# Optimization experiments

Hardware: AMD Instinct MI355X
Metric: run time of the kernel (lower is better)

## Reference

```python
import jax, jax.numpy as jnp
import numpy as np

D_MODEL = 512
NUM_HEADS = 8
DEPTH = D_MODEL // NUM_HEADS
BATCH = 2
SEQ = 2048
NEG_INF_SCALE = -1e9


def setup_inputs() -> dict:
    key = jax.random.key(0)
    ks = jax.random.split(key, 9)
    s = 0.02
    return {
        "v": jax.random.normal(ks[0], (BATCH, SEQ, D_MODEL), jnp.float32),
        "q": jax.random.normal(ks[1], (BATCH, SEQ, D_MODEL), jnp.float32),
        "k": jax.random.normal(ks[2], (BATCH, SEQ, D_MODEL), jnp.float32),
        "mask": jax.random.randint(ks[3], (BATCH, 1, SEQ, SEQ), 0, 2, jnp.int32),
        "wq_w": jax.random.normal(ks[4], (D_MODEL, D_MODEL), jnp.float32) * s,
        "wq_b": jnp.zeros((D_MODEL,), jnp.float32),
        "wk_w": jax.random.normal(ks[5], (D_MODEL, D_MODEL), jnp.float32) * s,
        "wk_b": jnp.zeros((D_MODEL,), jnp.float32),
        "wv_w": jax.random.normal(ks[6], (D_MODEL, D_MODEL), jnp.float32) * s,
        "wv_b": jnp.zeros((D_MODEL,), jnp.float32),
        "wo_w": jax.random.normal(ks[7], (D_MODEL, D_MODEL), jnp.float32) * s,
        "wo_b": jnp.zeros((D_MODEL,), jnp.float32),
    }


def _split_heads(x, b):
    # [b, s, d_model] -> [b, h, s, depth]
    return x.reshape(b, -1, NUM_HEADS, DEPTH).transpose(0, 2, 1, 3)


def reference(v, q, k, mask, wq_w, wq_b, wk_w, wk_b, wv_w, wv_b, wo_w, wo_b):
    b = q.shape[0]
    vv = _split_heads(v @ wv_w + wv_b, b)  # [b,h,s,d]
    kk = _split_heads(k @ wk_w + wk_b, b)
    qq = _split_heads(q @ wq_w + wq_b, b)
    # NOTE: the original code swaps q/k at the helper call site, so logits = K @ Q^T.
    logits = jnp.einsum("bhkd,bhqd->bhkq", kk, qq) / jnp.sqrt(jnp.float32(DEPTH))
    logits = logits + mask.astype(jnp.float32) * NEG_INF_SCALE
    attn = jax.nn.softmax(logits, axis=-1)  # softmax over the query axis (faithful quirk)
    # output = A^T @ V  -> [b,h,q,d]
    out = jnp.einsum("bhkq,bhkd->bhqd", attn, vv)
    concat = out.transpose(0, 2, 1, 3).reshape(b, -1, D_MODEL)
    return concat @ wo_w + wo_b, attn
```

## Files before the change

### kernel.cpp

```cpp
#include <hip/hip_runtime.h>

#define S 2048
#define DM 512
#define NH 8
#define HD 64
#define NB 2
#define BH (NB * NH)
#define MROWS (NB * S)

typedef __bf16 bf16x8 __attribute__((ext_vector_type(8)));
typedef float f32x4 __attribute__((ext_vector_type(4)));

union FragU {
  uint4 u;
  bf16x8 v;
  unsigned short s[8];
};

__device__ __forceinline__ unsigned short f2bf(float x) {
  unsigned u = __float_as_uint(x);
  u += 0x7FFFu + ((u >> 16) & 1u);
  return (unsigned short)(u >> 16);
}

__global__ void k_wtrans(const float* __restrict__ w0, const float* __restrict__ w1,
                         const float* __restrict__ w2, const float* __restrict__ w3,
                         unsigned short* __restrict__ wt) {
  __shared__ float tile[64][65];
  int i = blockIdx.z;
  const float* w = (i == 0) ? w0 : (i == 1) ? w1 : (i == 2) ? w2 : w3;
  int k0 = blockIdx.x * 64;
  int n0 = blockIdx.y * 64;
  int tx = threadIdx.x, ty = threadIdx.y;
  for (int r = ty; r < 64; r += 4)
    tile[r][tx] = w[(size_t)(k0 + r) * DM + n0 + tx];
  __syncthreads();
  unsigned short* o = wt + (size_t)i * DM * DM;
  for (int r = ty; r < 64; r += 4)
    o[(size_t)(n0 + r) * DM + k0 + tx] = f2bf(tile[tx][r]);
}

__global__ __launch_bounds__(256) void k_proj(
    const float* __restrict__ inq, const float* __restrict__ ink, const float* __restrict__ inv,
    const unsigned short* __restrict__ wt,
    const float* __restrict__ bq, const float* __restrict__ bk, const float* __restrict__ bv,
    unsigned short* __restrict__ oq, unsigned short* __restrict__ ok, unsigned short* __restrict__ ov) {
  int which = blockIdx.z;
  const float* in = (which == 0) ? inq : (which == 1) ? ink : inv;
  const float* bias = (which == 0) ? bq : (which == 1) ? bk : bv;
  unsigned short* out = (which == 0) ? oq : (which == 1) ? ok : ov;
  const unsigned short* w = wt + (size_t)which * DM * DM;

  int lane = threadIdx.x & 63, wv = threadIdx.x >> 6;
  int m0 = blockIdx.x * 64 + wv * 16;
  int n0 = blockIdx.y * 64;
  int kf = (lane >> 4) * 8;
  int arow = m0 + (lane & 15);

  f32x4 acc[4] = {{0.f, 0.f, 0.f, 0.f}, {0.f, 0.f, 0.f, 0.f},
                  {0.f, 0.f, 0.f, 0.f}, {0.f, 0.f, 0.f, 0.f}};

  for (int kk0 = 0; kk0 < DM; kk0 += 32) {
    const float* ap = in + (size_t)arow * DM + kk0 + kf;
    float4 a0 = *(const float4*)ap;
    float4 a1 = *(const float4*)(ap + 4);
    FragU af;
    af.s[0] = f2bf(a0.x); af.s[1] = f2bf(a0.y); af.s[2] = f2bf(a0.z); af.s[3] = f2bf(a0.w);
    af.s[4] = f2bf(a1.x); af.s[5] = f2bf(a1.y); af.s[6] = f2bf(a1.z); af.s[7] = f2bf(a1.w);
#pragma unroll
    for (int nt = 0; nt < 4; nt++) {
      FragU bfr;
      bfr.u = *(const uint4*)(w + (size_t)(n0 + nt * 16 + (lane & 15)) * DM + kk0 + kf);
      acc[nt] = __builtin_amdgcn_mfma_f32_16x16x32_bf16(af.v, bfr.v, acc[nt], 0, 0, 0);
    }
  }
#pragma unroll
  for (int nt = 0; nt < 4; nt++) {
#pragma unroll
    for (int r = 0; r < 4; r++) {
      int row = m0 + (lane >> 4) * 4 + r;
      int col = n0 + nt * 16 + (lane & 15);
      float val = acc[nt][r] + bias[col];
      int b = row >> 11, sIdx = row & (S - 1);
      int h = col >> 6, d = col & 63;
      out[(((size_t)(b * NH + h) * S) + sIdx) * HD + d] = f2bf(val);
    }
  }
}

__global__ void k_vtrans(const unsigned short* __restrict__ vin, unsigned short* __restrict__ vout) {
  __shared__ unsigned short tile[64][65];
  int bh = blockIdx.y;
  int s0 = blockIdx.x * 64;
  int tx = threadIdx.x, ty = threadIdx.y;
  const unsigned short* ip = vin + (size_t)bh * S * HD;
  for (int r = ty; r < 64; r += 4)
    tile[r][tx] = ip[(size_t)(s0 + r) * HD + tx];
  __syncthreads();
  unsigned short* op = vout + (size_t)bh * S * HD;
  for (int r = ty; r < 64; r += 4)
    op[(size_t)r * S + s0 + tx] = tile[tx][r];
}

__global__ __launch_bounds__(256) void k_softmax_z(
    const unsigned short* __restrict__ qq, const unsigned short* __restrict__ kk,
    const int* __restrict__ mask, float* __restrict__ invZ) {
  int lane = threadIdx.x & 63, w = threadIdx.x >> 6;
  int bh = blockIdx.y;
  int b = bh >> 3;
  int k0 = blockIdx.x * 64 + w * 16;
  int kf = (lane >> 4) * 8;

  const unsigned short* kbase = kk + ((size_t)bh * S + k0 + (lane & 15)) * HD + kf;
  FragU a0, a1;
  a0.u = *(const uint4*)kbase;
  a1.u = *(const uint4*)(kbase + 32);

  const unsigned short* qbase = qq + (size_t)bh * S * HD;
  const int* mrow = mask + (size_t)b * S * S;

  float sum[4] = {0.f, 0.f, 0.f, 0.f};

  for (int q0 = 0; q0 < S; q0 += 64) {
#pragma unroll
    for (int nt = 0; nt < 4; nt++) {
      int qcol = q0 + nt * 16 + (lane & 15);
      const unsigned short* qp = qbase + (size_t)qcol * HD + kf;
      FragU b0, b1;
      b0.u = *(const uint4*)qp;
      b1.u = *(const uint4*)(qp + 32);
      f32x4 c = {0.f, 0.f, 0.f, 0.f};
      c = __builtin_amdgcn_mfma_f32_16x16x32_bf16(a0.v, b0.v, c, 0, 0, 0);
      c = __builtin_amdgcn_mfma_f32_16x16x32_bf16(a1.v, b1.v, c, 0, 0, 0);
#pragma unroll
      for (int r = 0; r < 4; r++) {
        int krow = k0 + (lane >> 4) * 4 + r;
        int msk = mrow[(size_t)krow * S + qcol];
        float e = __expf(c[r] * 0.125f);
        sum[r] += msk ? 0.f : e;
      }
    }
  }
#pragma unroll
  for (int r = 0; r < 4; r++) {
    float s = sum[r];
    s += __shfl_xor(s, 1);
    s += __shfl_xor(s, 2);
    s += __shfl_xor(s, 4);
    s += __shfl_xor(s, 8);
    if ((lane & 15) == 0)
      invZ[(size_t)bh * S + k0 + (lane >> 4) * 4 + r] = 1.0f / s;
  }
}

__global__ __launch_bounds__(256) void k_attn(
    const unsigned short* __restrict__ qq, const unsigned short* __restrict__ kk,
    const unsigned short* __restrict__ vvT, const int* __restrict__ mask,
    const float* __restrict__ invZ, float* __restrict__ attn_out,
    unsigned short* __restrict__ concat) {
  __shared__ __align__(16) unsigned short pT[64][72];
  int lane = threadIdx.x & 63, w = threadIdx.x >> 6;
  int bh = blockIdx.y;
  int b = bh >> 3, h = bh & 7;
  int q0 = blockIdx.x * 64;
  int kf = (lane >> 4) * 8;

  FragU bq[4][2];
#pragma unroll
  for (int nt = 0; nt < 4; nt++) {
    const unsigned short* qp = qq + ((size_t)bh * S + q0 + nt * 16 + (lane & 15)) * HD + kf;
    bq[nt][0].u = *(const uint4*)qp;
    bq[nt][1].u = *(const uint4*)(qp + 32);
  }

  f32x4 o[4] = {{0.f, 0.f, 0.f, 0.f}, {0.f, 0.f, 0.f, 0.f},
                {0.f, 0.f, 0.f, 0.f}, {0.f, 0.f, 0.f, 0.f}};

  const unsigned short* kkb = kk + (size_t)bh * S * HD;
  const unsigned short* vb = vvT + (size_t)bh * HD * S;
  const int* mrow = mask + (size_t)b * S * S;
  float* ao = attn_out + (size_t)bh * S * S;
  const float* izb = invZ + (size_t)bh * S;

  for (int k0 = 0; k0 < S; k0 += 64) {
    int kw = k0 + w * 16;
    const unsigned short* kp = kkb + (size_t)(kw + (lane & 15)) * HD + kf;
    FragU a0, a1;
    a0.u = *(const uint4*)kp;
    a1.u = *(const uint4*)(kp + 32);
    float iz[4];
#pragma unroll
    for (int r = 0; r < 4; r++) iz[r] = izb[kw + (lane >> 4) * 4 + r];

#pragma unroll
    for (int nt = 0; nt < 4; nt++) {
      f32x4 c = {0.f, 0.f, 0.f, 0.f};
      c = __builtin_amdgcn_mfma_f32_16x16x32_bf16(a0.v, bq[nt][0].v, c, 0, 0, 0);
      c = __builtin_amdgcn_mfma_f32_16x16x32_bf16(a1.v, bq[nt][1].v, c, 0, 0, 0);
      int ql = nt * 16 + (lane & 15);
      int qcol = q0 + ql;
#pragma unroll
      for (int r = 0; r < 4; r++) {
        int kl = w * 16 + (lane >> 4) * 4 + r;
        int krow = k0 + kl;
        int msk = mrow[(size_t)krow * S + qcol];
        float a = msk ? 0.f : __expf(c[r] * 0.125f) * iz[r];
        ao[(size_t)krow * S + qcol] = a;
        pT[ql][kl] = f2bf(a);
      }
    }
    __syncthreads();

#pragma unroll
    for (int ks = 0; ks < 2; ks++) {
      FragU af;
      af.u = *(const uint4*)(&pT[w * 16 + (lane & 15)][kf + ks * 32]);
#pragma unroll
      for (int nt = 0; nt < 4; nt++) {
        FragU bfr;
        bfr.u = *(const uint4*)(vb + (size_t)(nt * 16 + (lane & 15)) * S + k0 + kf + ks * 32);
        o[nt] = __builtin_amdgcn_mfma_f32_16x16x32_bf16(af.v, bfr.v, o[nt], 0, 0, 0);
      }
    }
    __syncthreads();
  }

#pragma unroll
  for (int nt = 0; nt < 4; nt++) {
#pragma unroll
    for (int r = 0; r < 4; r++) {
      int qg = q0 + w * 16 + (lane >> 4) * 4 + r;
      int col = h * 64 + nt * 16 + (lane & 15);
      concat[((size_t)b * S + qg) * DM + col] = f2bf(o[nt][r]);
    }
  }
}

__global__ __launch_bounds__(256) void k_outproj(
    const unsigned short* __restrict__ concat, const unsigned short* __restrict__ wt,
    const float* __restrict__ bias, float* __restrict__ out) {
  const unsigned short* w = wt + (size_t)3 * DM * DM;
  int lane = threadIdx.x & 63, wv = threadIdx.x >> 6;
  int m0 = blockIdx.x * 64 + wv * 16;
  int n0 = blockIdx.y * 64;
  int kf = (lane >> 4) * 8;

  f32x4 acc[4] = {{0.f, 0.f, 0.f, 0.f}, {0.f, 0.f, 0.f, 0.f},
                  {0.f, 0.f, 0.f, 0.f}, {0.f, 0.f, 0.f, 0.f}};

  for (int kk0 = 0; kk0 < DM; kk0 += 32) {
    FragU af;
    af.u = *(const uint4*)(concat + (size_t)(m0 + (lane & 15)) * DM + kk0 + kf);
#pragma unroll
    for (int nt = 0; nt < 4; nt++) {
      FragU bfr;
      bfr.u = *(const uint4*)(w + (size_t)(n0 + nt * 16 + (lane & 15)) * DM + kk0 + kf);
      acc[nt] = __builtin_amdgcn_mfma_f32_16x16x32_bf16(af.v, bfr.v, acc[nt], 0, 0, 0);
    }
  }
#pragma unroll
  for (int nt = 0; nt < 4; nt++) {
#pragma unroll
    for (int r = 0; r < 4; r++) {
      int row = m0 + (lane >> 4) * 4 + r;
      int col = n0 + nt * 16 + (lane & 15);
      out[(size_t)row * DM + col] = acc[nt][r] + bias[col];
    }
  }
}

extern "C" void kernel_launch(void* const* d_in, const int* in_sizes, int n_in,
                              void* d_out, int out_size, void* d_ws, size_t ws_size,
                              hipStream_t stream) {
  (void)in_sizes; (void)n_in; (void)out_size; (void)ws_size;
  const float* v    = (const float*)d_in[0];
  const float* q    = (const float*)d_in[1];
  const float* k    = (const float*)d_in[2];
  const int*   mask = (const int*)d_in[3];
  const float* wq_w = (const float*)d_in[4];
  const float* wq_b = (const float*)d_in[5];
  const float* wk_w = (const float*)d_in[6];
  const float* wk_b = (const float*)d_in[7];
  const float* wv_w = (const float*)d_in[8];
  const float* wv_b = (const float*)d_in[9];
  const float* wo_w = (const float*)d_in[10];
  const float* wo_b = (const float*)d_in[11];

  char* ws = (char*)d_ws;
  size_t off = 0;
  auto alloc = [&](size_t bytes) {
    char* p = ws + off;
    off += (bytes + 255) & ~(size_t)255;
    return p;
  };
  unsigned short* wt   = (unsigned short*)alloc((size_t)4 * DM * DM * 2);
  unsigned short* qq   = (unsigned short*)alloc((size_t)BH * S * HD * 2);
  unsigned short* kk2  = (unsigned short*)alloc((size_t)BH * S * HD * 2);
  unsigned short* vstd = (unsigned short*)alloc((size_t)BH * S * HD * 2);
  unsigned short* vvT  = (unsigned short*)alloc((size_t)BH * S * HD * 2);
  float*          invZ = (float*)alloc((size_t)BH * S * 4);
  unsigned short* conc = (unsigned short*)alloc((size_t)MROWS * DM * 2);

  float* out_final = (float*)d_out;
  float* out_attn  = (float*)d_out + (size_t)MROWS * DM;

  k_wtrans<<<dim3(8, 8, 4), dim3(64, 4), 0, stream>>>(wq_w, wk_w, wv_w, wo_w, wt);
  k_proj<<<dim3(64, 8, 3), 256, 0, stream>>>(q, k, v, wt, wq_b, wk_b, wv_b, qq, kk2, vstd);
  k_vtrans<<<dim3(32, 16), dim3(64, 4), 0, stream>>>(vstd, vvT);
  k_softmax_z<<<dim3(32, 16), 256, 0, stream>>>(qq, kk2, mask, invZ);
  k_attn<<<dim3(32, 16), 256, 0, stream>>>(qq, kk2, vvT, mask, invZ, out_attn, conc);
  k_outproj<<<dim3(64, 8), 256, 0, stream>>>(conc, wt, wo_b, out_final);
}
```

Baseline: 573.3 us.

## Bit-pack mask, pre-convert inputs to bf16, split softmax and attention along keys

Adds a pass that packs the int32 mask into bitmasks, so the softmax-normalizer and attention kernels read 1 bit per element instead of 4 bytes. Inputs are converted to bf16 once before projection. Both attention-side kernels now split their reduction axis in two along blockIdx.z to double the grid: the normalizer uses atomicAdd partial sums plus a reciprocal kernel, and the attention kernel writes fp32 partial outputs that a reduce kernel sums into bf16. This costs extra launches and extra traffic for the partial buffers.

Measured after the change: 576.4 us. About the same (+0.6%).

```diff
diff --git a/kernel.cpp b/kernel.cpp
--- a/kernel.cpp
+++ b/kernel.cpp
@@ -7,6 +7,7 @@
 #define NB 2
 #define BH (NB * NH)
 #define MROWS (NB * S)
+#define QW (S / 32)
 
 typedef __bf16 bf16x8 __attribute__((ext_vector_type(8)));
 typedef float f32x4 __attribute__((ext_vector_type(4)));
@@ -40,13 +41,40 @@
     o[(size_t)(n0 + r) * DM + k0 + tx] = f2bf(tile[tx][r]);
 }
 
+__global__ __launch_bounds__(256) void k_cvt(
+    const float* __restrict__ q, const float* __restrict__ k, const float* __restrict__ v,
+    unsigned short* __restrict__ oq, unsigned short* __restrict__ ok, unsigned short* __restrict__ ov) {
+  int which = blockIdx.y;
+  const float* src = (which == 0) ? q : (which == 1) ? k : v;
+  unsigned short* dst = (which == 0) ? oq : (which == 1) ? ok : ov;
+  size_t t = (size_t)blockIdx.x * 256 + threadIdx.x;
+  const float4* s4 = (const float4*)src + t * 2;
+  float4 x = s4[0], y = s4[1];
+  FragU f;
+  f.s[0] = f2bf(x.x); f.s[1] = f2bf(x.y); f.s[2] = f2bf(x.z); f.s[3] = f2bf(x.w);
+  f.s[4] = f2bf(y.x); f.s[5] = f2bf(y.y); f.s[6] = f2bf(y.z); f.s[7] = f2bf(y.w);
+  *(uint4*)(dst + t * 8) = f.u;
+}
+
+__global__ __launch_bounds__(256) void k_maskpack(const int* __restrict__ mask,
+                                                  unsigned* __restrict__ mp) {
+  size_t gid = (size_t)blockIdx.x * 256 + threadIdx.x;
+  int m = mask[gid];
+  unsigned long long bal = __ballot(m != 0);
+  int lane = threadIdx.x & 63;
+  if (lane == 0) {
+    uint2 wds = make_uint2((unsigned)bal, (unsigned)(bal >> 32));
+    *(uint2*)&mp[gid >> 5] = wds;
+  }
+}
+
 __global__ __launch_bounds__(256) void k_proj(
-    const float* __restrict__ inq, const float* __restrict__ ink, const float* __restrict__ inv,
-    const unsigned short* __restrict__ wt,
+    const unsigned short* __restrict__ inq, const unsigned short* __restrict__ ink,
+    const unsigned short* __restrict__ inv, const unsigned short* __restrict__ wt,
     const float* __restrict__ bq, const float* __restrict__ bk, const float* __restrict__ bv,
     unsigned short* __restrict__ oq, unsigned short* __restrict__ ok, unsigned short* __restrict__ ov) {
   int which = blockIdx.z;
-  const float* in = (which == 0) ? inq : (which == 1) ? ink : inv;
+  const unsigned short* in = (which == 0) ? inq : (which == 1) ? ink : inv;
   const float* bias = (which == 0) ? bq : (which == 1) ? bk : bv;
   unsigned short* out = (which == 0) ? oq : (which == 1) ? ok : ov;
   const unsigned short* w = wt + (size_t)which * DM * DM;
@@ -61,12 +89,8 @@
                   {0.f, 0.f, 0.f, 0.f}, {0.f, 0.f, 0.f, 0.f}};
 
   for (int kk0 = 0; kk0 < DM; kk0 += 32) {
-    const float* ap = in + (size_t)arow * DM + kk0 + kf;
-    float4 a0 = *(const float4*)ap;
-    float4 a1 = *(const float4*)(ap + 4);
     FragU af;
-    af.s[0] = f2bf(a0.x); af.s[1] = f2bf(a0.y); af.s[2] = f2bf(a0.z); af.s[3] = f2bf(a0.w);
-    af.s[4] = f2bf(a1.x); af.s[5] = f2bf(a1.y); af.s[6] = f2bf(a1.z); af.s[7] = f2bf(a1.w);
+    af.u = *(const uint4*)(in + (size_t)arow * DM + kk0 + kf);
 #pragma unroll
     for (int nt = 0; nt < 4; nt++) {
       FragU bfr;
@@ -102,42 +126,48 @@
     op[(size_t)r * S + s0 + tx] = tile[tx][r];
 }
 
-__global__ __launch_bounds__(256) void k_softmax_z(
+__global__ __launch_bounds__(256, 4) void k_softmax_z(
     const unsigned short* __restrict__ qq, const unsigned short* __restrict__ kk,
-    const int* __restrict__ mask, float* __restrict__ invZ) {
+    const unsigned* __restrict__ mp, float* __restrict__ Zsum) {
   int lane = threadIdx.x & 63, w = threadIdx.x >> 6;
   int bh = blockIdx.y;
   int b = bh >> 3;
   int k0 = blockIdx.x * 64 + w * 16;
   int kf = (lane >> 4) * 8;
+  int qbase = blockIdx.z * (S / 2);
+  int krow_b = k0 + (lane >> 4) * 4;
 
   const unsigned short* kbase = kk + ((size_t)bh * S + k0 + (lane & 15)) * HD + kf;
   FragU a0, a1;
   a0.u = *(const uint4*)kbase;
   a1.u = *(const uint4*)(kbase + 32);
 
-  const unsigned short* qbase = qq + (size_t)bh * S * HD;
-  const int* mrow = mask + (size_t)b * S * S;
+  const unsigned short* qbaseP = qq + (size_t)bh * S * HD;
+  const unsigned* mpb = mp + (size_t)b * S * QW;
 
   float sum[4] = {0.f, 0.f, 0.f, 0.f};
 
-  for (int q0 = 0; q0 < S; q0 += 64) {
+  for (int q0 = qbase; q0 < qbase + S / 2; q0 += 64) {
+    uint2 mw[4];
+#pragma unroll
+    for (int r = 0; r < 4; r++)
+      mw[r] = *(const uint2*)&mpb[(size_t)(krow_b + r) * QW + (q0 >> 5)];
 #pragma unroll
     for (int nt = 0; nt < 4; nt++) {
       int qcol = q0 + nt * 16 + (lane & 15);
-      const unsigned short* qp = qbase + (size_t)qcol * HD + kf;
+      const unsigned short* qp = qbaseP + (size_t)qcol * HD + kf;
       FragU b0, b1;
       b0.u = *(const uint4*)qp;
       b1.u = *(const uint4*)(qp + 32);
       f32x4 c = {0.f, 0.f, 0.f, 0.f};
       c = __builtin_amdgcn_mfma_f32_16x16x32_bf16(a0.v, b0.v, c, 0, 0, 0);
       c = __builtin_amdgcn_mfma_f32_16x16x32_bf16(a1.v, b1.v, c, 0, 0, 0);
+      unsigned bpos = (unsigned)(nt * 16 + (lane & 15)) & 31u;
 #pragma unroll
       for (int r = 0; r < 4; r++) {
-        int krow = k0 + (lane >> 4) * 4 + r;
-        int msk = mrow[(size_t)krow * S + qcol];
+        unsigned word = (nt < 2) ? mw[r].x : mw[r].y;
         float e = __expf(c[r] * 0.125f);
-        sum[r] += msk ? 0.f : e;
+        sum[r] += ((word >> bpos) & 1u) ? 0.f : e;
       }
     }
   }
@@ -149,20 +179,26 @@
     s += __shfl_xor(s, 4);
     s += __shfl_xor(s, 8);
     if ((lane & 15) == 0)
-      invZ[(size_t)bh * S + k0 + (lane >> 4) * 4 + r] = 1.0f / s;
-  }
-}
-
-__global__ __launch_bounds__(256) void k_attn(
+      atomicAdd(&Zsum[(size_t)bh * S + krow_b + r], s);
+  }
+}
+
+__global__ __launch_bounds__(256) void k_invz(float* __restrict__ z) {
+  int t = blockIdx.x * 256 + threadIdx.x;
+  z[t] = 1.0f / z[t];
+}
+
+__global__ __launch_bounds__(256, 4) void k_attn(
     const unsigned short* __restrict__ qq, const unsigned short* __restrict__ kk,
-    const unsigned short* __restrict__ vvT, const int* __restrict__ mask,
+    const unsigned short* __restrict__ vvT, const unsigned* __restrict__ mp,
     const float* __restrict__ invZ, float* __restrict__ attn_out,
-    unsigned short* __restrict__ concat) {
+    float* __restrict__ pO) {
   __shared__ __align__(16) unsigned short pT[64][72];
   int lane = threadIdx.x & 63, w = threadIdx.x >> 6;
   int bh = blockIdx.y;
   int b = bh >> 3, h = bh & 7;
   int q0 = blockIdx.x * 64;
+  int kbase = blockIdx.z * (S / 2);
   int kf = (lane >> 4) * 8;
 
   FragU bq[4][2];
@@ -178,19 +214,25 @@
 
   const unsigned short* kkb = kk + (size_t)bh * S * HD;
   const unsigned short* vb = vvT + (size_t)bh * HD * S;
-  const int* mrow = mask + (size_t)b * S * S;
+  const unsigned* mpb = mp + (size_t)b * S * QW;
   float* ao = attn_out + (size_t)bh * S * S;
   const float* izb = invZ + (size_t)bh * S;
-
-  for (int k0 = 0; k0 < S; k0 += 64) {
+  int q0w = q0 >> 5;
+
+  for (int k0 = kbase; k0 < kbase + S / 2; k0 += 64) {
     int kw = k0 + w * 16;
+    int krow_b = kw + (lane >> 4) * 4;
     const unsigned short* kp = kkb + (size_t)(kw + (lane & 15)) * HD + kf;
     FragU a0, a1;
     a0.u = *(const uint4*)kp;
     a1.u = *(const uint4*)(kp + 32);
     float iz[4];
-#pragma unroll
-    for (int r = 0; r < 4; r++) iz[r] = izb[kw + (lane >> 4) * 4 + r];
+    uint2 mw[4];
+#pragma unroll
+    for (int r = 0; r < 4; r++) {
+      iz[r] = izb[krow_b + r];
+      mw[r] = *(const uint2*)&mpb[(size_t)(krow_b + r) * QW + q0w];
+    }
 
 #pragma unroll
     for (int nt = 0; nt < 4; nt++) {
@@ -199,12 +241,13 @@
       c = __builtin_amdgcn_mfma_f32_16x16x32_bf16(a1.v, bq[nt][1].v, c, 0, 0, 0);
       int ql = nt * 16 + (lane & 15);
       int qcol = q0 + ql;
+      unsigned bpos = (unsigned)ql & 31u;
 #pragma unroll
       for (int r = 0; r < 4; r++) {
         int kl = w * 16 + (lane >> 4) * 4 + r;
         int krow = k0 + kl;
-        int msk = mrow[(size_t)krow * S + qcol];
-        float a = msk ? 0.f : __expf(c[r] * 0.125f) * iz[r];
+        unsigned word = (nt < 2) ? mw[r].x : mw[r].y;
+        float a = ((word >> bpos) & 1u) ? 0.f : __expf(c[r] * 0.125f) * iz[r];
         ao[(size_t)krow * S + qcol] = a;
         pT[ql][kl] = f2bf(a);
       }
@@ -225,15 +268,30 @@
     __syncthreads();
   }
 
+  float* pOz = pO + (size_t)blockIdx.z * MROWS * DM;
 #pragma unroll
   for (int nt = 0; nt < 4; nt++) {
 #pragma unroll
     for (int r = 0; r < 4; r++) {
       int qg = q0 + w * 16 + (lane >> 4) * 4 + r;
       int col = h * 64 + nt * 16 + (lane & 15);
-      concat[((size_t)b * S + qg) * DM + col] = f2bf(o[nt][r]);
-    }
-  }
+      pOz[((size_t)b * S + qg) * DM + col] = o[nt][r];
+    }
+  }
+}
+
+__global__ __launch_bounds__(256) void k_reduceO(const float* __restrict__ p0,
+                                                  const float* __restrict__ p1,
+                                                  unsigned short* __restrict__ conc) {
+  size_t t = (size_t)blockIdx.x * 256 + threadIdx.x;
+  float4 a = ((const float4*)p0)[t];
+  float4 b = ((const float4*)p1)[t];
+  union { unsigned short s[4]; uint2 u; } o;
+  o.s[0] = f2bf(a.x + b.x);
+  o.s[1] = f2bf(a.y + b.y);
+  o.s[2] = f2bf(a.z + b.z);
+  o.s[3] = f2bf(a.w + b.w);
+  *(uint2*)(conc + t * 4) = o.u;
 }
 
 __global__ __launch_bounds__(256) void k_outproj(
@@ -294,20 +352,30 @@
     return p;
   };
   unsigned short* wt   = (unsigned short*)alloc((size_t)4 * DM * DM * 2);
+  unsigned short* qbf  = (unsigned short*)alloc((size_t)MROWS * DM * 2);
+  unsigned short* kbf  = (unsigned short*)alloc((size_t)MROWS * DM * 2);
+  unsigned short* vbf  = (unsigned short*)alloc((size_t)MROWS * DM * 2);
   unsigned short* qq   = (unsigned short*)alloc((size_t)BH * S * HD * 2);
   unsigned short* kk2  = (unsigned short*)alloc((size_t)BH * S * HD * 2);
   unsigned short* vstd = (unsigned short*)alloc((size_t)BH * S * HD * 2);
   unsigned short* vvT  = (unsigned short*)alloc((size_t)BH * S * HD * 2);
-  float*          invZ = (float*)alloc((size_t)BH * S * 4);
+  unsigned*       mp   = (unsigned*)alloc((size_t)NB * S * QW * 4);
+  float*          Zs   = (float*)alloc((size_t)BH * S * 4);
+  float*          pO   = (float*)alloc((size_t)2 * MROWS * DM * 4);
   unsigned short* conc = (unsigned short*)alloc((size_t)MROWS * DM * 2);
 
   float* out_final = (float*)d_out;
   float* out_attn  = (float*)d_out + (size_t)MROWS * DM;
 
   k_wtrans<<<dim3(8, 8, 4), dim3(64, 4), 0, stream>>>(wq_w, wk_w, wv_w, wo_w, wt);
-  k_proj<<<dim3(64, 8, 3), 256, 0, stream>>>(q, k, v, wt, wq_b, wk_b, wv_b, qq, kk2, vstd);
+  k_cvt<<<dim3(1024, 3), 256, 0, stream>>>(q, k, v, qbf, kbf, vbf);
+  k_maskpack<<<dim3(32768), 256, 0, stream>>>(mask, mp);
+  hipMemsetAsync(Zs, 0, (size_t)BH * S * 4, stream);
+  k_proj<<<dim3(64, 8, 3), 256, 0, stream>>>(qbf, kbf, vbf, wt, wq_b, wk_b, wv_b, qq, kk2, vstd);
   k_vtrans<<<dim3(32, 16), dim3(64, 4), 0, stream>>>(vstd, vvT);
-  k_softmax_z<<<dim3(32, 16), 256, 0, stream>>>(qq, kk2, mask, invZ);
-  k_attn<<<dim3(32, 16), 256, 0, stream>>>(qq, kk2, vvT, mask, invZ, out_attn, conc);
+  k_softmax_z<<<dim3(32, 16, 2), 256, 0, stream>>>(qq, kk2, mp, Zs);
+  k_invz<<<dim3(128), 256, 0, stream>>>(Zs);
+  k_attn<<<dim3(32, 16, 2), 256, 0, stream>>>(qq, kk2, vvT, mp, Zs, out_attn, pO);
+  k_reduceO<<<dim3(2048), 256, 0, stream>>>(pO, pO + (size_t)MROWS * DM, conc);
   k_outproj<<<dim3(64, 8), 256, 0, stream>>>(conc, wt, wo_b, out_final);
 }
```
